# Kernel tuning notes

Hardware: AMD Instinct MI355X
Metric: run time of the kernel (lower is better)

The kernel has to match this reference:

```python
import jax, jax.numpy as jnp
import numpy as np
from itertools import combinations_with_replacement

MAX_DEGREE = 4
INPUT_DIM = 16
BATCH = 32768

# Static gather-index tables: one [n_terms_d, d] int array per degree d.
IDX = {d: np.asarray(list(combinations_with_replacement(range(INPUT_DIM), d)), dtype=np.int32)
       for d in range(1, MAX_DEGREE + 1)}
P = 1 + sum(IDX[d].shape[0] for d in IDX)  # total polynomial features (4845)


def setup_inputs() -> dict:
    key = jax.random.key(0)
    k1, k2 = jax.random.split(key)
    x = jax.random.normal(k1, (BATCH, INPUT_DIM), dtype=jnp.float32)
    W = jax.random.normal(k2, (1, P), dtype=jnp.float32) * 0.02
    b = jnp.zeros((1,), dtype=jnp.float32)
    M_raw = jnp.zeros((), dtype=jnp.float32)
    return {"x": x, "W": W, "b": b, "M_raw": M_raw}


def _transform(x, M_raw):
    # M = sigmoid(M_raw) * (max_degree - 1) + 1  (soft degree threshold)
    M = jax.nn.sigmoid(M_raw) * (MAX_DEGREE - 1) + 1.0
    feats = [jnp.ones((x.shape[0], 1), dtype=x.dtype)]  # bias/constant term
    for d in range(1, MAX_DEGREE + 1):
        w = jax.nn.sigmoid(10.0 * (M - d + 0.5))  # per-degree soft weight
        idx = IDX[d]  # [n_d, d]
        prod = x[:, idx[:, 0]]  # [B, n_d]
        for j in range(1, d):  # small fixed loop over degree, not data dims
            prod = prod * x[:, idx[:, j]]
        feats.append(prod * w)
    return jnp.concatenate(feats, axis=1)  # [B, P]


def reference(x, W, b, M_raw):
    xt = _transform(x, M_raw)               # [B, P]
    logits = xt @ W.T + b                   # [B, 1]
    return jax.nn.sigmoid(logits)
```

## Files before the change

kernel.cpp:

```cpp
#include <hip/hip_runtime.h>
#include <math.h>

#define DIMS 16
#define BATCH 32768

__device__ constexpr int cnt2(int j){ return 16 - j; }
__device__ constexpr int cnt3(int j){ return (16 - j) * (17 - j) / 2; }
__device__ constexpr int cnt4(int j){ return (16 - j) * (17 - j) * (18 - j) / 6; }
__device__ constexpr int off2(int i0){ int s = 0; for (int j = 0; j < i0; ++j) s += cnt2(j); return s; }
__device__ constexpr int off3(int i0){ int s = 0; for (int j = 0; j < i0; ++j) s += cnt3(j); return s; }
__device__ constexpr int off4(int i0){ int s = 0; for (int j = 0; j < i0; ++j) s += cnt4(j); return s; }

template<int I0>
__device__ __forceinline__ void do_i0(const float* __restrict__ W,
                                      const float* __restrict__ xv,
                                      float& a1, float& a2, float& a3, float& a4)
{
    const float x0 = xv[I0];
    a1 = fmaf(W[1 + I0], x0, a1);
    int k2 = 17  + off2(I0);
    int k3 = 153 + off3(I0);
    int k4 = 969 + off4(I0);
    #pragma unroll
    for (int i1 = I0; i1 < DIMS; ++i1) {
        const float p2 = x0 * xv[i1];
        a2 = fmaf(W[k2++], p2, a2);
        #pragma unroll
        for (int i2 = i1; i2 < DIMS; ++i2) {
            const float p3 = p2 * xv[i2];
            a3 = fmaf(W[k3++], p3, a3);
            float s4 = 0.0f;
            #pragma unroll
            for (int i3 = i2; i3 < DIMS; ++i3)
                s4 = fmaf(W[k4++], xv[i3], s4);
            a4 = fmaf(p3, s4, a4);
        }
    }
}

template<int... Is>
__device__ __forceinline__ float role_partial(const float* __restrict__ W,
                                              const float* __restrict__ xv,
                                              float w1, float w2, float w3, float w4)
{
    float a1 = 0.f, a2 = 0.f, a3 = 0.f, a4 = 0.f;
    (do_i0<Is>(W, xv, a1, a2, a3, a4), ...);
    return fmaf(w1, a1, fmaf(w2, a2, fmaf(w3, a3, w4 * a4)));
}

__global__ __launch_bounds__(256, 2)
void poly_logreg_kernel(const float* __restrict__ x,
                        const float* __restrict__ W,
                        const float* __restrict__ b,
                        const float* __restrict__ M_raw,
                        float* __restrict__ out)
{
    const int lane = threadIdx.x & 63;
    const int wave = threadIdx.x >> 6;
    const int s    = (blockIdx.x << 6) + lane;

    const float M  = 3.0f / (1.0f + __expf(-M_raw[0])) + 1.0f;
    const float w1 = 1.0f / (1.0f + __expf(-10.0f * (M - 1.0f + 0.5f)));
    const float w2 = 1.0f / (1.0f + __expf(-10.0f * (M - 2.0f + 0.5f)));
    const float w3 = 1.0f / (1.0f + __expf(-10.0f * (M - 3.0f + 0.5f)));
    const float w4 = 1.0f / (1.0f + __expf(-10.0f * (M - 4.0f + 0.5f)));

    float xv[DIMS];
    const float4* xp = reinterpret_cast<const float4*>(x + (size_t)s * DIMS);
    #pragma unroll
    for (int q = 0; q < 4; ++q) {
        const float4 v = xp[q];
        xv[q * 4 + 0] = v.x; xv[q * 4 + 1] = v.y;
        xv[q * 4 + 2] = v.z; xv[q * 4 + 3] = v.w;
    }

    float partial;
    if (wave == 0)      partial = role_partial<0, 6>(W, xv, w1, w2, w3, w4);
    else if (wave == 1) partial = role_partial<1, 5, 13, 14, 15>(W, xv, w1, w2, w3, w4);
    else if (wave == 2) partial = role_partial<2, 4, 11, 12>(W, xv, w1, w2, w3, w4);
    else                partial = role_partial<3, 7, 8, 9, 10>(W, xv, w1, w2, w3, w4);

    __shared__ float part_lds[3][64];
    if (wave > 0) part_lds[wave - 1][lane] = partial;
    __syncthreads();

    if (wave == 0) {
        const float logit = W[0] + b[0] + partial
                          + part_lds[0][lane] + part_lds[1][lane] + part_lds[2][lane];
        out[s] = 1.0f / (1.0f + __expf(-logit));
    }
}

extern "C" void kernel_launch(void* const* d_in, const int* in_sizes, int n_in,
                              void* d_out, int out_size, void* d_ws, size_t ws_size,
                              hipStream_t stream)
{
    const float* x     = (const float*)d_in[0];
    const float* W     = (const float*)d_in[1];
    const float* b     = (const float*)d_in[2];
    const float* M_raw = (const float*)d_in[3];
    float* out = (float*)d_out;

    const int blocks = BATCH / 64;
    poly_logreg_kernel<<<blocks, 256, 0, stream>>>(x, W, b, M_raw, out);
}
```

Measured before the change: 13.29 us.

## Split work over 8 waves by (i0,i1) pairs with compile-time load balancing

Per-sample polynomial work is now split across 8 waves per block instead of 4. Work is assigned per (i0,i1) pair using a constexpr greedy balancing plan, rather than per leading index. The degree-3 sum is also refactored into a factored inner sum, which cuts multiplies. The intent is a shorter critical path per sample and more waves resident, at the cost of twice the threads per block, extra LDS reduction and larger code.

```diff
diff --git a/kernel.cpp b/kernel.cpp
--- a/kernel.cpp
+++ b/kernel.cpp
@@ -1,54 +1,130 @@
 #include <hip/hip_runtime.h>
+#include <utility>
 #include <math.h>
 
-#define DIMS 16
+#define DIMS  16
 #define BATCH 32768
+#define NPAIR 136
+#define NROLE 8
 
-__device__ constexpr int cnt2(int j){ return 16 - j; }
-__device__ constexpr int cnt3(int j){ return (16 - j) * (17 - j) / 2; }
-__device__ constexpr int cnt4(int j){ return (16 - j) * (17 - j) * (18 - j) / 6; }
-__device__ constexpr int off2(int i0){ int s = 0; for (int j = 0; j < i0; ++j) s += cnt2(j); return s; }
-__device__ constexpr int off3(int i0){ int s = 0; for (int j = 0; j < i0; ++j) s += cnt3(j); return s; }
-__device__ constexpr int off4(int i0){ int s = 0; for (int j = 0; j < i0; ++j) s += cnt4(j); return s; }
+constexpr int pairlex(int i0, int i1) {
+    int s = 0;
+    for (int j = 0; j < i0; ++j) s += (DIMS - j);
+    return s + (i1 - i0);
+}
+constexpr int cnt3(int j) { return (DIMS - j) * (DIMS + 1 - j) / 2; }
+constexpr int cnt4(int j) { return (DIMS - j) * (DIMS + 1 - j) * (DIMS + 2 - j) / 6; }
+constexpr int off3(int i0) { int s = 0; for (int j = 0; j < i0; ++j) s += cnt3(j); return s; }
+constexpr int off4(int i0) { int s = 0; for (int j = 0; j < i0; ++j) s += cnt4(j); return s; }
 
-template<int I0>
-__device__ __forceinline__ void do_i0(const float* __restrict__ W,
-                                      const float* __restrict__ xv,
-                                      float& a1, float& a2, float& a3, float& a4)
-{
-    const float x0 = xv[I0];
-    a1 = fmaf(W[1 + I0], x0, a1);
-    int k2 = 17  + off2(I0);
-    int k3 = 153 + off3(I0);
-    int k4 = 969 + off4(I0);
-    #pragma unroll
-    for (int i1 = I0; i1 < DIMS; ++i1) {
-        const float p2 = x0 * xv[i1];
-        a2 = fmaf(W[k2++], p2, a2);
-        #pragma unroll
-        for (int i2 = i1; i2 < DIMS; ++i2) {
-            const float p3 = p2 * xv[i2];
-            a3 = fmaf(W[k3++], p3, a3);
-            float s4 = 0.0f;
-            #pragma unroll
-            for (int i3 = i2; i3 < DIMS; ++i3)
-                s4 = fmaf(W[k4++], xv[i3], s4);
-            a4 = fmaf(p3, s4, a4);
+constexpr int w2idx(int i0, int i1) { return 1 + DIMS + pairlex(i0, i1); }
+constexpr int w3base(int i0, int i1) {
+    int s = off3(i0);
+    for (int b = i0; b < i1; ++b) s += (DIMS - b);
+    return 1 + DIMS + NPAIR + s;
+}
+constexpr int w4base(int i0, int i1) {
+    int s = off4(i0);
+    for (int b = i0; b < i1; ++b) s += cnt3(b);
+    return 1 + DIMS + NPAIR + 816 + s;
+}
+static_assert(pairlex(15, 15) == 135, "pairlex");
+static_assert(off3(DIMS) == 816 && off4(DIMS) == 3876, "counts");
+static_assert(w3base(15, 15) == 968, "w3 tail");
+static_assert(w4base(15, 15) == 4844, "w4 tail");
+
+constexpr int costv(int v) { return (DIMS - v) + (DIMS + 1 - v) * (DIMS + 2 - v) / 2 + 3; }
+
+struct Plan { int role_of[NPAIR]; int d1_role; };
+constexpr Plan make_plan() {
+    Plan p{};
+    long load[NROLE] = {};
+    for (int v = 0; v < DIMS; ++v)
+        for (int i0 = 0; i0 <= v; ++i0) {
+            int best = 0;
+            for (int r = 1; r < NROLE; ++r) if (load[r] < load[best]) best = r;
+            p.role_of[pairlex(i0, v)] = best;
+            load[best] += costv(v);
         }
-    }
+    int best = 0;
+    for (int r = 1; r < NROLE; ++r) if (load[r] < load[best]) best = r;
+    p.d1_role = best;
+    return p;
+}
+inline constexpr Plan PLAN = make_plan();
+
+constexpr int pid_i0(int pid) {
+    int i0 = 0, rem = pid;
+    while (rem >= DIMS - i0) { rem -= DIMS - i0; ++i0; }
+    return i0;
+}
+constexpr int pid_i1(int pid) {
+    int i0 = 0, rem = pid;
+    while (rem >= DIMS - i0) { rem -= DIMS - i0; ++i0; }
+    return i0 + rem;
 }
 
-template<int... Is>
-__device__ __forceinline__ float role_partial(const float* __restrict__ W,
-                                              const float* __restrict__ xv,
-                                              float w1, float w2, float w3, float w4)
+template<typename F, int... Is>
+__device__ __forceinline__ void static_for_impl(F&& f, std::integer_sequence<int, Is...>) {
+    (f(std::integral_constant<int, Is>{}), ...);
+}
+template<int N, typename F>
+__device__ __forceinline__ void static_for(F&& f) {
+    static_for_impl(static_cast<F&&>(f), std::make_integer_sequence<int, N>{});
+}
+
+template<int I0, int I1>
+__device__ __forceinline__ void do_pair(const float* __restrict__ W,
+                                        const float* __restrict__ xv,
+                                        float& a2, float& a3, float& a4)
+{
+    constexpr int KW2 = w2idx(I0, I1);
+    constexpr int KW3 = w3base(I0, I1);
+    constexpr int KW4 = w4base(I0, I1);
+
+    const float p2 = xv[I0] * xv[I1];
+    a2 = fmaf(W[KW2], p2, a2);
+
+    float s3 = 0.f;
+    #pragma unroll
+    for (int i2 = I1; i2 < DIMS; ++i2)
+        s3 = fmaf(W[KW3 + (i2 - I1)], xv[i2], s3);
+    a3 = fmaf(p2, s3, a3);
+
+    float t = 0.f;
+    int k = KW4;
+    #pragma unroll
+    for (int i2 = I1; i2 < DIMS; ++i2) {
+        float s4 = 0.f;
+        #pragma unroll
+        for (int i3 = i2; i3 < DIMS; ++i3)
+            s4 = fmaf(W[k++], xv[i3], s4);
+        t = fmaf(xv[i2], s4, t);
+    }
+    a4 = fmaf(p2, t, a4);
+}
+
+template<int R>
+__device__ __forceinline__ float role_body(const float* __restrict__ W,
+                                           const float* __restrict__ xv,
+                                           float w1, float w2, float w3, float w4)
 {
     float a1 = 0.f, a2 = 0.f, a3 = 0.f, a4 = 0.f;
-    (do_i0<Is>(W, xv, a1, a2, a3, a4), ...);
+    static_for<NPAIR>([&](auto K) {
+        constexpr int pid = decltype(K)::value;
+        if constexpr (PLAN.role_of[pid] == R) {
+            do_pair<pid_i0(pid), pid_i1(pid)>(W, xv, a2, a3, a4);
+        }
+    });
+    if constexpr (R == PLAN.d1_role) {
+        #pragma unroll
+        for (int i = 0; i < DIMS; ++i)
+            a1 = fmaf(W[1 + i], xv[i], a1);
+    }
     return fmaf(w1, a1, fmaf(w2, a2, fmaf(w3, a3, w4 * a4)));
 }
 
-__global__ __launch_bounds__(256, 2)
+__global__ __launch_bounds__(512, 4)
 void poly_logreg_kernel(const float* __restrict__ x,
                         const float* __restrict__ W,
                         const float* __restrict__ b,
@@ -60,10 +136,10 @@
     const int s    = (blockIdx.x << 6) + lane;
 
     const float M  = 3.0f / (1.0f + __expf(-M_raw[0])) + 1.0f;
-    const float w1 = 1.0f / (1.0f + __expf(-10.0f * (M - 1.0f + 0.5f)));
-    const float w2 = 1.0f / (1.0f + __expf(-10.0f * (M - 2.0f + 0.5f)));
-    const float w3 = 1.0f / (1.0f + __expf(-10.0f * (M - 3.0f + 0.5f)));
-    const float w4 = 1.0f / (1.0f + __expf(-10.0f * (M - 4.0f + 0.5f)));
+    const float w1 = 1.0f / (1.0f + __expf(-10.0f * (M - 0.5f)));
+    const float w2 = 1.0f / (1.0f + __expf(-10.0f * (M - 1.5f)));
+    const float w3 = 1.0f / (1.0f + __expf(-10.0f * (M - 2.5f)));
+    const float w4 = 1.0f / (1.0f + __expf(-10.0f * (M - 3.5f)));
 
     float xv[DIMS];
     const float4* xp = reinterpret_cast<const float4*>(x + (size_t)s * DIMS);
@@ -75,18 +151,25 @@
     }
 
     float partial;
-    if (wave == 0)      partial = role_partial<0, 6>(W, xv, w1, w2, w3, w4);
-    else if (wave == 1) partial = role_partial<1, 5, 13, 14, 15>(W, xv, w1, w2, w3, w4);
-    else if (wave == 2) partial = role_partial<2, 4, 11, 12>(W, xv, w1, w2, w3, w4);
-    else                partial = role_partial<3, 7, 8, 9, 10>(W, xv, w1, w2, w3, w4);
+    switch (wave) {
+        case 0:  partial = role_body<0>(W, xv, w1, w2, w3, w4); break;
+        case 1:  partial = role_body<1>(W, xv, w1, w2, w3, w4); break;
+        case 2:  partial = role_body<2>(W, xv, w1, w2, w3, w4); break;
+        case 3:  partial = role_body<3>(W, xv, w1, w2, w3, w4); break;
+        case 4:  partial = role_body<4>(W, xv, w1, w2, w3, w4); break;
+        case 5:  partial = role_body<5>(W, xv, w1, w2, w3, w4); break;
+        case 6:  partial = role_body<6>(W, xv, w1, w2, w3, w4); break;
+        default: partial = role_body<7>(W, xv, w1, w2, w3, w4); break;
+    }
 
-    __shared__ float part_lds[3][64];
-    if (wave > 0) part_lds[wave - 1][lane] = partial;
+    __shared__ float red[NROLE - 1][64];
+    if (wave) red[wave - 1][lane] = partial;
     __syncthreads();
 
     if (wave == 0) {
-        const float logit = W[0] + b[0] + partial
-                          + part_lds[0][lane] + part_lds[1][lane] + part_lds[2][lane];
+        float logit = W[0] + b[0] + partial;
+        #pragma unroll
+        for (int w = 0; w < NROLE - 1; ++w) logit += red[w][lane];
         out[s] = 1.0f / (1.0f + __expf(-logit));
     }
 }
@@ -102,5 +185,5 @@
     float* out = (float*)d_out;
 
     const int blocks = BATCH / 64;
-    poly_logreg_kernel<<<blocks, 256, 0, stream>>>(x, W, b, M_raw, out);
+    poly_logreg_kernel<<<blocks, 512, 0, stream>>>(x, W, b, M_raw, out);
 }
```

Measured after the change: 12.59 us. 5.3% less time.
